# Kernel optimization log

Hardware: AMD Instinct MI355X
Metric: run time of the kernel (lower is better)

The kernel has to match this reference:

```python
import jax, jax.numpy as jnp
import numpy as np

D = 1024
N = 50000
SCALE = 1.0 / D  # scale torch.rand-style params to keep exp() in range


def _attention_module(X, W_alpha, a_alpha, b_alpha, W_sum):
    # a_w, b_w: [1, D] row vectors (a_alpha.T @ W_alpha)
    a_w = a_alpha[:, 0] @ W_alpha  # [D]
    b_w = b_alpha[:, 0] @ W_alpha  # [D]
    # score_j = a_w . X[0] + b_w . X[j]  -> alpha_j = exp(score_j)
    scores = jnp.dot(a_w, X[0]) + X @ b_w  # [N]
    alpha = jnp.exp(scores)  # [N]
    # weighted sum over neighbors, normalized by total alpha
    sum_output = (alpha @ X) / jnp.sum(alpha)  # [D]
    return sum_output @ W_sum  # [D]


def setup_inputs() -> dict:
    key = jax.random.key(0)
    ks = jax.random.split(key, 12)
    rand = lambda k, shape: jax.random.uniform(k, shape, dtype=jnp.float32) * SCALE
    return {
        "X_in": jax.random.normal(ks[0], (N, D), dtype=jnp.float32),
        "X_out": jax.random.normal(ks[1], (N, D), dtype=jnp.float32),
        "W_alpha_in": rand(ks[2], (D, D)),
        "a_alpha_in": rand(ks[3], (D, 1)),
        "b_alpha_in": rand(ks[4], (D, 1)),
        "W_sum_in": rand(ks[5], (D, D)),
        "W_alpha_out": rand(ks[6], (D, D)),
        "a_alpha_out": rand(ks[7], (D, 1)),
        "b_alpha_out": rand(ks[8], (D, 1)),
        "W_sum_out": rand(ks[9], (D, D)),
        "lin_W": jax.random.normal(ks[10], (D, 2 * D), dtype=jnp.float32) / np.sqrt(2 * D),
        "lin_b": jnp.zeros((D,), dtype=jnp.float32),
    }


def reference(X_in, X_out, W_alpha_in, a_alpha_in, b_alpha_in, W_sum_in,
              W_alpha_out, a_alpha_out, b_alpha_out, W_sum_out, lin_W, lin_b):
    res_in = _attention_module(X_in, W_alpha_in, a_alpha_in, b_alpha_in, W_sum_in)    # [D]
    res_out = _attention_module(X_out, W_alpha_out, a_alpha_out, b_alpha_out, W_sum_out)  # [D]
    attn = jnp.concatenate([res_in, res_out], axis=0)  # [2D]
    return jax.nn.elu(attn @ lin_W.T + lin_b)  # [D]
```

## Files before the change

### kernel.cpp

```cpp
#include <hip/hip_runtime.h>
#include <math.h>


#define DD 1024
#define NROWS 50000
#define GB 1024
#define RB 4
#define NPART 32

__global__ __launch_bounds__(256) void vecmat_partial(
    const float* __restrict__ v0, const float* __restrict__ M0,
    const float* __restrict__ v1, const float* __restrict__ M1,
    float* __restrict__ out) {
  int bid = blockIdx.x;
  int module = bid >> 7;
  int r = bid & 127;
  int jb = r & 3;
  int ic = r >> 2;
  const float* __restrict__ v = module ? v1 : v0;
  const float* __restrict__ M = module ? M1 : M0;
  int j = jb * 256 + threadIdx.x;
  int i0 = ic * 32;
  float acc = 0.f;
#pragma unroll 8
  for (int i = i0; i < i0 + 32; ++i)
    acc = fmaf(v[i], M[i * DD + j], acc);
  atomicAdd(&out[module * DD + j], acc);
}

__global__ __launch_bounds__(256, 8) void attn_pass(
    const float* __restrict__ X0, const float* __restrict__ X1,
    const float* __restrict__ bw_all,
    float* __restrict__ num_part,
    float* __restrict__ den_part) {
  int bid = blockIdx.x;
  int module = (bid >= GB) ? 1 : 0;
  int b = module ? bid - GB : bid;
  const float* __restrict__ X = module ? X1 : X0;
  const float* __restrict__ bw = bw_all + module * DD;

  int tid = threadIdx.x;
  int lane = tid & 63;
  int wave = tid >> 6;
  int w = b * 4 + wave;
  const int WPM = GB * 4;

  float4 bwv[4], acc[4];
#pragma unroll
  for (int q = 0; q < 4; ++q) {
    bwv[q] = *reinterpret_cast<const float4*>(&bw[q * 256 + lane * 4]);
    acc[q] = make_float4(0.f, 0.f, 0.f, 0.f);
  }
  float asum = 0.f;

  for (int j0 = w * RB; j0 < NROWS; j0 += WPM * RB) {
    float4 xv[RB][4];
#pragma unroll
    for (int r = 0; r < RB; ++r) {
      const float4* __restrict__ row =
          reinterpret_cast<const float4*>(X + (size_t)(j0 + r) * DD);
#pragma unroll
      for (int q = 0; q < 4; ++q) xv[r][q] = row[q * 64 + lane];
    }
    float s[RB];
#pragma unroll
    for (int r = 0; r < RB; ++r) {
      float t = 0.f;
#pragma unroll
      for (int q = 0; q < 4; ++q) {
        t = fmaf(xv[r][q].x, bwv[q].x, t);
        t = fmaf(xv[r][q].y, bwv[q].y, t);
        t = fmaf(xv[r][q].z, bwv[q].z, t);
        t = fmaf(xv[r][q].w, bwv[q].w, t);
      }
      s[r] = t;
    }
#pragma unroll
    for (int off = 32; off >= 1; off >>= 1) {
#pragma unroll
      for (int r = 0; r < RB; ++r) s[r] += __shfl_xor(s[r], off, 64);
    }
#pragma unroll
    for (int r = 0; r < RB; ++r) {
      float alpha = __expf(s[r]);
      asum += alpha;
#pragma unroll
      for (int q = 0; q < 4; ++q) {
        acc[q].x = fmaf(alpha, xv[r][q].x, acc[q].x);
        acc[q].y = fmaf(alpha, xv[r][q].y, acc[q].y);
        acc[q].z = fmaf(alpha, xv[r][q].z, acc[q].z);
        acc[q].w = fmaf(alpha, xv[r][q].w, acc[q].w);
      }
    }
  }

  __shared__ float sdata[4][DD];
  __shared__ float dsum[4];
#pragma unroll
  for (int q = 0; q < 4; ++q)
    *reinterpret_cast<float4*>(&sdata[wave][q * 256 + lane * 4]) = acc[q];
  if (lane == 0) dsum[wave] = asum;
  __syncthreads();

  float4 a0 = *reinterpret_cast<float4*>(&sdata[0][tid * 4]);
  float4 a1 = *reinterpret_cast<float4*>(&sdata[1][tid * 4]);
  float4 a2 = *reinterpret_cast<float4*>(&sdata[2][tid * 4]);
  float4 a3 = *reinterpret_cast<float4*>(&sdata[3][tid * 4]);
  int p = module * NPART + (b & (NPART - 1));
  float* __restrict__ np = num_part + (size_t)p * DD;
  int c = tid * 4;
  atomicAdd(&np[c + 0], a0.x + a1.x + a2.x + a3.x);
  atomicAdd(&np[c + 1], a0.y + a1.y + a2.y + a3.y);
  atomicAdd(&np[c + 2], a0.z + a1.z + a2.z + a3.z);
  atomicAdd(&np[c + 3], a0.w + a1.w + a2.w + a3.w);
  if (tid == 0) atomicAdd(&den_part[p], dsum[0] + dsum[1] + dsum[2] + dsum[3]);
}

__global__ __launch_bounds__(256) void reduce_partials(
    const float* __restrict__ num_part, const float* __restrict__ den_part,
    float* __restrict__ num, float* __restrict__ den) {
  int idx = blockIdx.x * 256 + threadIdx.x;
  int m = idx >> 10;
  int i = idx & (DD - 1);
  float s = 0.f;
#pragma unroll
  for (int p = 0; p < NPART; ++p)
    s += num_part[((size_t)(m * NPART + p)) * DD + i];
  num[idx] = s;
  if (idx < 2) {
    float d = 0.f;
#pragma unroll
    for (int p = 0; p < NPART; ++p) d += den_part[idx * NPART + p];
    den[idx] = d;
  }
}

__global__ __launch_bounds__(256) void final_kernel(
    const float* __restrict__ res_raw, const float* __restrict__ den,
    const float* __restrict__ linW, const float* __restrict__ linb,
    float* __restrict__ out) {
  int k = blockIdx.x;
  int tid = threadIdx.x;
  float inv0 = 1.f / den[0];
  float inv1 = 1.f / den[1];
  const float* __restrict__ row = linW + (size_t)k * (2 * DD);
  float acc = 0.f;
#pragma unroll
  for (int s = 0; s < 8; ++s) {
    int m = s * 256 + tid;
    float attn = res_raw[m] * (m < DD ? inv0 : inv1);
    acc = fmaf(attn, row[m], acc);
  }
#pragma unroll
  for (int off = 32; off >= 1; off >>= 1) acc += __shfl_xor(acc, off, 64);
  __shared__ float wsum[4];
  int lane = tid & 63, wave = tid >> 6;
  if (lane == 0) wsum[wave] = acc;
  __syncthreads();
  if (tid == 0) {
    float v = wsum[0] + wsum[1] + wsum[2] + wsum[3] + linb[k];
    out[k] = v > 0.f ? v : expm1f(v);
  }
}

extern "C" void kernel_launch(void* const* d_in, const int* in_sizes, int n_in,
                              void* d_out, int out_size, void* d_ws, size_t ws_size,
                              hipStream_t stream) {
  const float* X_in    = (const float*)d_in[0];
  const float* X_out   = (const float*)d_in[1];
  const float* W_a_in  = (const float*)d_in[2];
  const float* b_a_in  = (const float*)d_in[4];
  const float* W_s_in  = (const float*)d_in[5];
  const float* W_a_out = (const float*)d_in[6];
  const float* b_a_out = (const float*)d_in[8];
  const float* W_s_out = (const float*)d_in[9];
  const float* linW    = (const float*)d_in[10];
  const float* linb    = (const float*)d_in[11];
  float* out = (float*)d_out;
  float* ws  = (float*)d_ws;

  float* bw       = ws;
  float* num_part = ws + 2048;
  float* den_part = ws + 67584;
  float* res_raw  = ws + 67648;
  float* num      = ws + 69696;
  float* den      = ws + 71744;

  hipMemsetAsync(d_ws, 0, 69696 * sizeof(float), stream);
  vecmat_partial<<<256, 256, 0, stream>>>(b_a_in, W_a_in, b_a_out, W_a_out, bw);
  attn_pass<<<2 * GB, 256, 0, stream>>>(X_in, X_out, bw, num_part, den_part);
  reduce_partials<<<8, 256, 0, stream>>>(num_part, den_part, num, den);
  vecmat_partial<<<256, 256, 0, stream>>>(num, W_s_in, num + 1024, W_s_out, res_raw);
  final_kernel<<<DD, 256, 0, stream>>>(res_raw, den, linW, linb, out);
}
```

Baseline: 497.3 us.

## Stage four contiguous X rows through shared memory per block iteration

Each block now loads four consecutive rows (16 KB contiguous) cooperatively into LDS, and each wave then processes one row from shared memory. Previously each wave loaded four rows directly into registers. The aim is more contiguous, coalesced global reads and fewer registers per thread. In exchange it adds two block-wide barriers per iteration and LDS traffic, and it removes the per-wave 4-row register batching that hid memory latency.

```diff
diff --git a/kernel.cpp b/kernel.cpp
--- a/kernel.cpp
+++ b/kernel.cpp
@@ -5,7 +5,6 @@
 #define DD 1024
 #define NROWS 50000
 #define GB 1024
-#define RB 4
 #define NPART 32
 
 __global__ __launch_bounds__(256) void vecmat_partial(
@@ -42,8 +41,9 @@
   int tid = threadIdx.x;
   int lane = tid & 63;
   int wave = tid >> 6;
-  int w = b * 4 + wave;
-  const int WPM = GB * 4;
+
+  __shared__ float stage[4][DD];
+  __shared__ float dsum[4];
 
   float4 bwv[4], acc[4];
 #pragma unroll
@@ -53,59 +53,52 @@
   }
   float asum = 0.f;
 
-  for (int j0 = w * RB; j0 < NROWS; j0 += WPM * RB) {
-    float4 xv[RB][4];
+  for (int c = b; c * 4 < NROWS; c += GB) {
+    int j0 = c * 4;
+    const float4* __restrict__ src =
+        reinterpret_cast<const float4*>(X + (size_t)j0 * DD);
+    float4 tmp[4];
 #pragma unroll
-    for (int r = 0; r < RB; ++r) {
-      const float4* __restrict__ row =
-          reinterpret_cast<const float4*>(X + (size_t)(j0 + r) * DD);
+    for (int r = 0; r < 4; ++r) tmp[r] = src[r * 256 + tid];
 #pragma unroll
-      for (int q = 0; q < 4; ++q) xv[r][q] = row[q * 64 + lane];
-    }
-    float s[RB];
+    for (int r = 0; r < 4; ++r)
+      *reinterpret_cast<float4*>(&stage[r][tid * 4]) = tmp[r];
+    __syncthreads();
+
+    float t = 0.f;
 #pragma unroll
-    for (int r = 0; r < RB; ++r) {
-      float t = 0.f;
-#pragma unroll
-      for (int q = 0; q < 4; ++q) {
-        t = fmaf(xv[r][q].x, bwv[q].x, t);
-        t = fmaf(xv[r][q].y, bwv[q].y, t);
-        t = fmaf(xv[r][q].z, bwv[q].z, t);
-        t = fmaf(xv[r][q].w, bwv[q].w, t);
-      }
-      s[r] = t;
+    for (int q = 0; q < 4; ++q) {
+      float4 xv = *reinterpret_cast<const float4*>(&stage[wave][q * 256 + lane * 4]);
+      t = fmaf(xv.x, bwv[q].x, t);
+      t = fmaf(xv.y, bwv[q].y, t);
+      t = fmaf(xv.z, bwv[q].z, t);
+      t = fmaf(xv.w, bwv[q].w, t);
     }
 #pragma unroll
-    for (int off = 32; off >= 1; off >>= 1) {
+    for (int off = 32; off >= 1; off >>= 1) t += __shfl_xor(t, off, 64);
+    float alpha = __expf(t);
+    asum += alpha;
 #pragma unroll
-      for (int r = 0; r < RB; ++r) s[r] += __shfl_xor(s[r], off, 64);
+    for (int q = 0; q < 4; ++q) {
+      float4 xv = *reinterpret_cast<const float4*>(&stage[wave][q * 256 + lane * 4]);
+      acc[q].x = fmaf(alpha, xv.x, acc[q].x);
+      acc[q].y = fmaf(alpha, xv.y, acc[q].y);
+      acc[q].z = fmaf(alpha, xv.z, acc[q].z);
+      acc[q].w = fmaf(alpha, xv.w, acc[q].w);
     }
-#pragma unroll
-    for (int r = 0; r < RB; ++r) {
-      float alpha = __expf(s[r]);
-      asum += alpha;
-#pragma unroll
-      for (int q = 0; q < 4; ++q) {
-        acc[q].x = fmaf(alpha, xv[r][q].x, acc[q].x);
-        acc[q].y = fmaf(alpha, xv[r][q].y, acc[q].y);
-        acc[q].z = fmaf(alpha, xv[r][q].z, acc[q].z);
-        acc[q].w = fmaf(alpha, xv[r][q].w, acc[q].w);
-      }
-    }
+    __syncthreads();
   }
 
-  __shared__ float sdata[4][DD];
-  __shared__ float dsum[4];
 #pragma unroll
   for (int q = 0; q < 4; ++q)
-    *reinterpret_cast<float4*>(&sdata[wave][q * 256 + lane * 4]) = acc[q];
+    *reinterpret_cast<float4*>(&stage[wave][q * 256 + lane * 4]) = acc[q];
   if (lane == 0) dsum[wave] = asum;
   __syncthreads();
 
-  float4 a0 = *reinterpret_cast<float4*>(&sdata[0][tid * 4]);
-  float4 a1 = *reinterpret_cast<float4*>(&sdata[1][tid * 4]);
-  float4 a2 = *reinterpret_cast<float4*>(&sdata[2][tid * 4]);
-  float4 a3 = *reinterpret_cast<float4*>(&sdata[3][tid * 4]);
+  float4 a0 = *reinterpret_cast<float4*>(&stage[0][tid * 4]);
+  float4 a1 = *reinterpret_cast<float4*>(&stage[1][tid * 4]);
+  float4 a2 = *reinterpret_cast<float4*>(&stage[2][tid * 4]);
+  float4 a3 = *reinterpret_cast<float4*>(&stage[3][tid * 4]);
   int p = module * NPART + (b & (NPART - 1));
   float* __restrict__ np = num_part + (size_t)p * DD;
   int c = tid * 4;
```

New measurement: 459.5 us. 7.6% less time.
